# Kernel tuning notes

Measured on AMD Instinct MI355X. Metric: run time of the kernel, lower is better.

The kernel has to match this reference:

```python
import jax, jax.numpy as jnp
import numpy as np

NUM_BASIC = 2
NUM_MIXED = 4
NUM_FRAME = 8
NUM_NODES = 7
CLIP_LEN = 8   # file-level constant in source
GROUP = 7      # file-level constant in source (== NUM_NODES)
N = 1 + NUM_NODES * NUM_FRAME          # 57
T = 2 * NUM_FRAME - 1                  # 15 temporal taps


def setup_inputs() -> dict:
    key = jax.random.key(0)
    k1, k2, k3 = jax.random.split(key, 3)
    # forward input: H x n x n basic pattern adjacency
    mat = jax.random.normal(k1, (NUM_BASIC, NUM_NODES, NUM_NODES), jnp.float32)
    # learned params
    temporal_expansion = jax.random.normal(k2, (NUM_MIXED, NUM_BASIC, T), jnp.float32)
    # per-mixer Linear(num_basic -> 1): weight (M, num_basic), bias (M,)
    mixer_w = jax.random.normal(k3, (NUM_MIXED, NUM_BASIC), jnp.float32) / np.sqrt(NUM_BASIC)
    mixer_b = jnp.zeros((NUM_MIXED,), jnp.float32)
    # mixed_mat parameter with its structured init (zeros, first col 0.5, row0 every GROUP-th = 1)
    mm = np.zeros((NUM_MIXED, N, N), np.float32)
    mm[:, :, 0] = 0.5
    mm[:, 0, ::GROUP] = 1.0
    mixed_mat_param = jnp.asarray(mm)
    return {"mat": mat, "temporal_expansion": temporal_expansion,
            "mixer_w": mixer_w, "mixer_b": mixer_b,
            "mixed_mat_param": mixed_mat_param}


def _forward(mat, temporal_expansion, mixer_w, mixer_b, mixed_mat_param):
    # sigmoid over temporal expansion: (M, B, T)
    exp = jax.nn.sigmoid(temporal_expansion)
    # einsum 'h t, h n m -> h t n m' per mixer, then rearrange 'h t n m -> n (t m) h'
    # -> (M, n, T*m, B)
    im = jnp.einsum('iht,hnm->intmh', exp, mat).reshape(NUM_MIXED, NUM_NODES, T * NUM_NODES, NUM_BASIC)
    # Linear(B->1) then ReLU (Rearrange is a pure permutation): (M, n, T*m)
    mixed = jax.nn.relu(jnp.einsum('intk,ik->int', im, mixer_w) + mixer_b[:, None, None])

    mm = mixed_mat_param
    # block scatter-adds: frame i's node rows get a sliding temporal window of `mixed`
    for i in range(CLIP_LEN):
        sl = mixed[:, :, NUM_NODES * (CLIP_LEN - 1 - i):NUM_NODES * (2 * CLIP_LEN - 1 - i)]  # (M,7,56)
        mm = mm.at[:, 1 + i * NUM_NODES:1 + (i + 1) * NUM_NODES, 1:].add(sl)

    # sparsify: for row r_i = (1+i)*GROUP, zero block-j columns (j != i) except col (1+j)*GROUP
    cols = jnp.arange(N)
    blk = jnp.arange(CLIP_LEN)
    own_block = (cols[None, :] >= 1 + GROUP * blk[:, None]) & (cols[None, :] <= GROUP * (blk[:, None] + 1))
    zero_mask = (cols[None, :] >= 1) & (cols[None, :] % GROUP != 0) & (~own_block)  # (8, N)
    row_idx = GROUP * (1 + blk)  # 7,14,...,56
    rows = mm[:, row_idx, :]     # (M, 8, N)
    mm = mm.at[:, row_idx, :].set(jnp.where(zero_mask[None, :, :], 0.0, rows))

    # symmetric normalization D^-1/2 A D^-1/2 with degree = clamped row sums
    d = jnp.maximum(jnp.sum(mm, axis=2), 1.0) ** -0.5  # (M, N)
    return d[:, :, None] * mm * d[:, None, :]


def reference(mat, temporal_expansion, mixer_w, mixer_b, mixed_mat_param):
    return _forward(mat, temporal_expansion, mixer_w, mixer_b, mixed_mat_param)
```

## Files before the change

kernel.cpp:

```cpp
#include <hip/hip_runtime.h>
#include <math.h>

#define NUM_MIXED 4
#define NN        57
#define TT        15

__global__ __launch_bounds__(256) void pattern_mixer_kernel(
    const float* __restrict__ mat,
    const float* __restrict__ te,
    const float* __restrict__ mixer_w,
    const float* __restrict__ mixer_b,
    const float* __restrict__ mmp,
    float* __restrict__ out)
{
    const int i   = blockIdx.x;
    const int tid = threadIdx.x;

    __shared__ float s_mat[2 * 49];
    __shared__ float s_sig[2 * TT];
    __shared__ float s_mixed[7 * 105];
    __shared__ float s_mm[NN * NN];
    __shared__ float s_d[NN];

    if (tid < 30) {
        float x = te[i * 30 + tid];
        s_sig[tid] = 1.0f / (1.0f + expf(-x));
    } else if (tid >= 32 && tid < 32 + 98) {
        s_mat[tid - 32] = mat[tid - 32];
    }
    __syncthreads();

    const float w0 = mixer_w[i * 2 + 0];
    const float w1 = mixer_w[i * 2 + 1];
    const float b  = mixer_b[i];
    for (int k = tid; k < 735; k += 256) {
        int n = k / 105;
        int c = k % 105;
        int t = c / 7;
        int m = c % 7;
        float v = fmaf(w0 * s_sig[t], s_mat[n * 7 + m],
                  fmaf(w1 * s_sig[TT + t], s_mat[49 + n * 7 + m], b));
        s_mixed[k] = fmaxf(v, 0.0f);
    }
    __syncthreads();

    if (tid < 228) {
        const int r = tid >> 2;
        const int q = tid & 3;
        const int iclip = (r - 1) / 7;
        const int n     = (r - 1) % 7;
        const bool maskrow = (r > 0) && (r % 7 == 0);
        const int blk = r / 7 - 1;
        const float* __restrict__ basep  = mmp + i * NN * NN + r * NN;
        const float* __restrict__ mixp   = s_mixed + n * 105 + 7 * (7 - iclip) - 1;

        float s = 0.0f;
        for (int c = q; c < NN; c += 4) {
            float v = basep[c];
            if (r >= 1 && c >= 1)
                v += mixp[c];
            if (maskrow) {
                bool own = (c >= 1 + 7 * blk) && (c <= 7 * blk + 7);
                if (c >= 1 && (c % 7) != 0 && !own)
                    v = 0.0f;
            }
            s_mm[r * NN + c] = v;
            s += v;
        }
        s += __shfl_xor(s, 1);
        s += __shfl_xor(s, 2);
        if (q == 0)
            s_d[r] = rsqrtf(fmaxf(s, 1.0f));
    }
    __syncthreads();

    float* __restrict__ outp = out + i * NN * NN;
    for (int k = tid; k < NN * NN; k += 256) {
        int r = k / NN;
        int c = k % NN;
        outp[k] = s_d[r] * s_mm[k] * s_d[c];
    }
}

extern "C" void kernel_launch(void* const* d_in, const int* in_sizes, int n_in,
                              void* d_out, int out_size, void* d_ws, size_t ws_size,
                              hipStream_t stream) {
    const float* mat     = (const float*)d_in[0];
    const float* te      = (const float*)d_in[1];
    const float* mixer_w = (const float*)d_in[2];
    const float* mixer_b = (const float*)d_in[3];
    const float* mmp     = (const float*)d_in[4];
    float* out           = (float*)d_out;

    pattern_mixer_kernel<<<NUM_MIXED, 256, 0, stream>>>(mat, te, mixer_w, mixer_b, mmp, out);
}
```

Before: 10.60 us.

## Compute mixed values in registers per thread, dropping shared staging and two barriers

Restructures the kernel so each of 456 threads owns one 7-column block of a row. Each thread computes its sigmoid-weighted mixer values directly in registers from global memory, applies the block mask, and reduces row sums with an 8-lane shuffle. This removes the shared-memory staging of sigmoid, mat, mixed and the full matrix, along with two __syncthreads. In exchange it repeats the exp and mat loads per thread and raises the block size to 512.

Measured after the change: 9.711 us. -8.4%, faster.

```diff
diff --git a/kernel.cpp b/kernel.cpp
--- a/kernel.cpp
+++ b/kernel.cpp
@@ -3,9 +3,8 @@
 
 #define NUM_MIXED 4
 #define NN        57
-#define TT        15
 
-__global__ __launch_bounds__(256) void pattern_mixer_kernel(
+__global__ __launch_bounds__(512) void pattern_mixer_kernel(
     const float* __restrict__ mat,
     const float* __restrict__ te,
     const float* __restrict__ mixer_w,
@@ -15,70 +14,69 @@
 {
     const int i   = blockIdx.x;
     const int tid = threadIdx.x;
+    const bool active = tid < 456;
+    const int r = tid >> 3;
+    const int q = tid & 7;
 
-    __shared__ float s_mat[2 * 49];
-    __shared__ float s_sig[2 * TT];
-    __shared__ float s_mixed[7 * 105];
-    __shared__ float s_mm[NN * NN];
     __shared__ float s_d[NN];
 
-    if (tid < 30) {
-        float x = te[i * 30 + tid];
-        s_sig[tid] = 1.0f / (1.0f + expf(-x));
-    } else if (tid >= 32 && tid < 32 + 98) {
-        s_mat[tid - 32] = mat[tid - 32];
-    }
-    __syncthreads();
+    float v[7];
+    float v0 = 0.0f;
 
-    const float w0 = mixer_w[i * 2 + 0];
-    const float w1 = mixer_w[i * 2 + 1];
-    const float b  = mixer_b[i];
-    for (int k = tid; k < 735; k += 256) {
-        int n = k / 105;
-        int c = k % 105;
-        int t = c / 7;
-        int m = c % 7;
-        float v = fmaf(w0 * s_sig[t], s_mat[n * 7 + m],
-                  fmaf(w1 * s_sig[TT + t], s_mat[49 + n * 7 + m], b));
-        s_mixed[k] = fmaxf(v, 0.0f);
-    }
-    __syncthreads();
+    if (active) {
+        const float* __restrict__ bp = mmp + i * NN * NN + r * NN;
+        float base[7];
+        #pragma unroll
+        for (int j = 0; j < 7; ++j) base[j] = bp[7 * q + 1 + j];
+        if (q == 0) v0 = bp[0];
 
-    if (tid < 228) {
-        const int r = tid >> 2;
-        const int q = tid & 3;
-        const int iclip = (r - 1) / 7;
-        const int n     = (r - 1) % 7;
-        const bool maskrow = (r > 0) && (r % 7 == 0);
-        const int blk = r / 7 - 1;
-        const float* __restrict__ basep  = mmp + i * NN * NN + r * NN;
-        const float* __restrict__ mixp   = s_mixed + n * 105 + 7 * (7 - iclip) - 1;
+        const bool rge1  = (r >= 1);
+        const int  n     = rge1 ? (r - 1) % 7 : 0;
+        const int  iclip = rge1 ? (r - 1) / 7 : 0;
+        const int  t     = (7 - iclip) + q;
 
-        float s = 0.0f;
-        for (int c = q; c < NN; c += 4) {
-            float v = basep[c];
-            if (r >= 1 && c >= 1)
-                v += mixp[c];
-            if (maskrow) {
-                bool own = (c >= 1 + 7 * blk) && (c <= 7 * blk + 7);
-                if (c >= 1 && (c % 7) != 0 && !own)
-                    v = 0.0f;
+        const float w0 = mixer_w[i * 2 + 0];
+        const float w1 = mixer_w[i * 2 + 1];
+        const float b  = mixer_b[i];
+        const float x0 = te[i * 30 + t];
+        const float x1 = te[i * 30 + 15 + t];
+        const float a0 = w0 / (1.0f + expf(-x0));
+        const float a1 = w1 / (1.0f + expf(-x1));
+
+        const bool maskrow = rge1 && ((r % 7) == 0);
+        const int  blk     = r / 7 - 1;
+        const bool zerome  = maskrow && (q != blk);
+
+        float s = v0;
+        #pragma unroll
+        for (int j = 0; j < 7; ++j) {
+            float val = base[j];
+            if (rge1) {
+                float mx = fmaf(a0, mat[n * 7 + j],
+                           fmaf(a1, mat[49 + n * 7 + j], b));
+                val += fmaxf(mx, 0.0f);
             }
-            s_mm[r * NN + c] = v;
-            s += v;
+            if (zerome && j != 6) val = 0.0f;
+            v[j] = val;
+            s += val;
         }
         s += __shfl_xor(s, 1);
         s += __shfl_xor(s, 2);
-        if (q == 0)
-            s_d[r] = rsqrtf(fmaxf(s, 1.0f));
+        s += __shfl_xor(s, 4);
+        if (q == 0) s_d[r] = rsqrtf(fmaxf(s, 1.0f));
     }
+
     __syncthreads();
 
-    float* __restrict__ outp = out + i * NN * NN;
-    for (int k = tid; k < NN * NN; k += 256) {
-        int r = k / NN;
-        int c = k % NN;
-        outp[k] = s_d[r] * s_mm[k] * s_d[c];
+    if (active) {
+        const float dr = s_d[r];
+        float* __restrict__ op = out + i * NN * NN + r * NN;
+        #pragma unroll
+        for (int j = 0; j < 7; ++j) {
+            int c = 7 * q + 1 + j;
+            op[c] = dr * v[j] * s_d[c];
+        }
+        if (q == 0) op[0] = dr * v0 * s_d[0];
     }
 }
 
@@ -92,5 +90,5 @@
     const float* mmp     = (const float*)d_in[4];
     float* out           = (float*)d_out;
 
-    pattern_mixer_kernel<<<NUM_MIXED, 256, 0, stream>>>(mat, te, mixer_w, mixer_b, mmp, out);
+    pattern_mixer_kernel<<<NUM_MIXED, 512, 0, stream>>>(mat, te, mixer_w, mixer_b, mmp, out);
 }
```
